# Optimization experiments

Measured on AMD Instinct MI355X. Metric: run time of the kernel, lower is better.

## Reference

```python
import jax, jax.numpy as jnp
import numpy as np

B, I, N = 1024, 128, 256
UNFOLDS = 6  # ode_solver_unfolds


def _sig(v, mu, sigma):
    # v: [B, D] -> [B, D, 1]; mu/sigma: [D, N] -> broadcast [B, D, N]
    return jax.nn.sigmoid(sigma * (v[..., None] - mu))


def setup_inputs() -> dict:
    key = jax.random.key(0)
    ks = jax.random.split(key, 12)
    u = lambda k, shape, lo, hi: jax.random.uniform(k, shape, jnp.float32, lo, hi)
    pm1 = lambda k, shape: (2.0 * jax.random.randint(k, shape, 0, 2) - 1.0).astype(jnp.float32)
    return {
        "inputs": jax.random.normal(ks[0], (B, I), jnp.float32),
        "state": jax.random.normal(ks[1], (B, N), jnp.float32) * 0.1,
        "input_w": jnp.ones((I,), jnp.float32),
        "input_b": jnp.zeros((I,), jnp.float32),
        "sensory_mu": u(ks[2], (I, N), 0.3, 0.8),
        "sensory_sigma": u(ks[3], (I, N), 3.0, 8.0),
        "sensory_W": u(ks[4], (I, N), 0.01, 1.0),
        "sensory_erev": pm1(ks[5], (I, N)),
        "mu": u(ks[6], (N, N), 0.3, 0.8),
        "sigma": u(ks[7], (N, N), 3.0, 8.0),
        "W": u(ks[8], (N, N), 0.01, 1.0),
        "erev": pm1(ks[9], (N, N)),
        "vleak": u(ks[10], (N,), -0.2, 0.2),
        "gleak": jnp.ones((N,), jnp.float32),   # gleak_init_min == gleak_init_max == 1.0
        "cm_t": jnp.full((N,), 0.5, jnp.float32),  # cm_init_min == cm_init_max == 0.5
    }


def reference(inputs, state, input_w, input_b, sensory_mu, sensory_sigma,
              sensory_W, sensory_erev, mu, sigma, W, erev, vleak, gleak, cm_t):
    # Affine input mapping
    x = inputs * input_w + input_b  # [B, I]
    # Sensory synapse activations (constant across unfolds)
    s_act = sensory_W * _sig(x, sensory_mu, sensory_sigma)  # [B, I, N]
    w_num_sensory = jnp.sum(s_act * sensory_erev, axis=1)   # [B, N]
    w_den_sensory = jnp.sum(s_act, axis=1)                  # [B, N]

    def step(v_pre, _):
        w_act = W * _sig(v_pre, mu, sigma)                  # [B, N, N]
        w_num = jnp.sum(w_act * erev, axis=1) + w_num_sensory
        w_den = jnp.sum(w_act, axis=1) + w_den_sensory
        numerator = cm_t * v_pre + gleak * vleak + w_num
        denominator = cm_t + gleak + w_den
        return numerator / denominator, None

    v_pre, _ = jax.lax.scan(step, state, None, length=UNFOLDS)
    # module returns (outputs, next_state) with outputs == next_state
    return v_pre
```

## Files before the change

kernel.cpp:

```cpp
#include <hip/hip_runtime.h>


#define LOG2E 1.44269504088896340f

constexpr int Bn = 1024;
constexpr int In = 128;
constexpr int Nn = 256;
constexpr int UNFOLDS = 6;

typedef float v2f __attribute__((ext_vector_type(2)));

#if __has_builtin(__builtin_amdgcn_exp2f)
#define EXP2F(x) __builtin_amdgcn_exp2f(x)
#else
#define EXP2F(x) __exp2f(x)
#endif
#if __has_builtin(__builtin_amdgcn_rcpf)
#define RCPF(x) __builtin_amdgcn_rcpf(x)
#else
#define RCPF(x) (1.0f / (x))
#endif

__global__ __launch_bounds__(256) void pack_kernel(
    const float* __restrict__ mu, const float* __restrict__ sigma,
    const float* __restrict__ W, const float* __restrict__ erev,
    const float* __restrict__ smu, const float* __restrict__ ssigma,
    const float* __restrict__ sW, const float* __restrict__ serev,
    float4* __restrict__ Prec, float4* __restrict__ Psen) {
    int idx = blockIdx.x * 256 + threadIdx.x;
    if (idx < Nn * Nn) {
        float s = sigma[idx], m = mu[idx], w = W[idx], e = erev[idx];
        Prec[idx] = make_float4(s * LOG2E, s * m * LOG2E, w, w * e);
        return;
    }
    int j = idx - Nn * Nn;
    if (j < In * Nn) {
        float s = ssigma[j], m = smu[j], w = sW[j], e = serev[j];
        Psen[j] = make_float4(s * LOG2E, s * m * LOG2E, w, w * e);
    }
}

__global__ __launch_bounds__(1024, 1) void ltc_fused_kernel(
    const float* __restrict__ inputs, const float* __restrict__ state,
    const float* __restrict__ input_w, const float* __restrict__ input_b,
    const float4* __restrict__ Psen, const float4* __restrict__ Prec,
    const float* __restrict__ vleak, const float* __restrict__ gleak,
    const float* __restrict__ cmt, float* __restrict__ out) {
    __shared__ float4 vt[Nn];
    __shared__ float2 part[4][4][Nn];
    __shared__ float4 xs[In];

    const int tid = threadIdx.x;
    const int b0 = blockIdx.x * 4;
    const int n = tid & 255;
    const int ih = tid >> 8;

    float vp = state[(b0 + ih) * Nn + n];
    ((float*)vt)[n * 4 + ih] = vp;
    if (tid < 4 * In) {
        int i = tid & 127, bb = tid >> 7;
        ((float*)xs)[i * 4 + bb] =
            inputs[(b0 + bb) * In + i] * input_w[i] + input_b[i];
    }
    const float g = gleak[n], c = cmt[n];
    const float gvl = g * vleak[n];
    __syncthreads();

    float sens_n, sens_d;
    {
        v2f acc0 = {0.f, 0.f}, acc1 = {0.f, 0.f};
        v2f acc2 = {0.f, 0.f}, acc3 = {0.f, 0.f};
        const float4* __restrict__ pp = Psen + n;
#pragma unroll 8
        for (int i = ih * 32; i < ih * 32 + 32; ++i) {
            float4 p = pp[i * Nn];
            float4 v = xs[i];
            v2f AA = {p.x, p.x};
            v2f BB = {p.y, p.y};
            v2f WW = {p.z, p.w};
            v2f u01 = __builtin_elementwise_fma(-AA, (v2f){v.x, v.y}, BB);
            v2f u23 = __builtin_elementwise_fma(-AA, (v2f){v.z, v.w}, BB);
            v2f a01 = (v2f){EXP2F(u01.x), EXP2F(u01.y)} + 1.0f;
            v2f a23 = (v2f){EXP2F(u23.x), EXP2F(u23.y)} + 1.0f;
            float r0 = RCPF(a01.x), r1 = RCPF(a01.y);
            float r2 = RCPF(a23.x), r3 = RCPF(a23.y);
            acc0 = __builtin_elementwise_fma(WW, (v2f){r0, r0}, acc0);
            acc1 = __builtin_elementwise_fma(WW, (v2f){r1, r1}, acc1);
            acc2 = __builtin_elementwise_fma(WW, (v2f){r2, r2}, acc2);
            acc3 = __builtin_elementwise_fma(WW, (v2f){r3, r3}, acc3);
        }
        part[ih][0][n] = make_float2(acc0.y, acc0.x);
        part[ih][1][n] = make_float2(acc1.y, acc1.x);
        part[ih][2][n] = make_float2(acc2.y, acc2.x);
        part[ih][3][n] = make_float2(acc3.y, acc3.x);
        __syncthreads();
        float wn = 0.f, wd = 0.f;
#pragma unroll
        for (int s = 0; s < 4; ++s) {
            float2 v = part[s][ih][n];
            wn += v.x;
            wd += v.y;
        }
        sens_n = wn;
        sens_d = wd;
    }

    const float4* __restrict__ pp = Prec + n;
    for (int s = 0; s < UNFOLDS; ++s) {
        __syncthreads();
        v2f acc0 = {0.f, 0.f}, acc1 = {0.f, 0.f};
        v2f acc2 = {0.f, 0.f}, acc3 = {0.f, 0.f};
#pragma unroll 8
        for (int i = ih * 64; i < ih * 64 + 64; ++i) {
            float4 p = pp[i * Nn];
            float4 v = vt[i];
            v2f AA = {p.x, p.x};
            v2f BB = {p.y, p.y};
            v2f WW = {p.z, p.w};
            v2f u01 = __builtin_elementwise_fma(-AA, (v2f){v.x, v.y}, BB);
            v2f u23 = __builtin_elementwise_fma(-AA, (v2f){v.z, v.w}, BB);
            v2f a01 = (v2f){EXP2F(u01.x), EXP2F(u01.y)} + 1.0f;
            v2f a23 = (v2f){EXP2F(u23.x), EXP2F(u23.y)} + 1.0f;
            float r0 = RCPF(a01.x), r1 = RCPF(a01.y);
            float r2 = RCPF(a23.x), r3 = RCPF(a23.y);
            acc0 = __builtin_elementwise_fma(WW, (v2f){r0, r0}, acc0);
            acc1 = __builtin_elementwise_fma(WW, (v2f){r1, r1}, acc1);
            acc2 = __builtin_elementwise_fma(WW, (v2f){r2, r2}, acc2);
            acc3 = __builtin_elementwise_fma(WW, (v2f){r3, r3}, acc3);
        }
        part[ih][0][n] = make_float2(acc0.y, acc0.x);
        part[ih][1][n] = make_float2(acc1.y, acc1.x);
        part[ih][2][n] = make_float2(acc2.y, acc2.x);
        part[ih][3][n] = make_float2(acc3.y, acc3.x);
        __syncthreads();
        float wn = sens_n, wd = sens_d;
#pragma unroll
        for (int s2 = 0; s2 < 4; ++s2) {
            float2 v = part[s2][ih][n];
            wn += v.x;
            wd += v.y;
        }
        float res = (c * vp + gvl + wn) * RCPF(c + g + wd);
        vp = res;
        if (s == UNFOLDS - 1)
            out[(b0 + ih) * Nn + n] = res;
        else
            ((float*)vt)[n * 4 + ih] = res;
    }
}

extern "C" void kernel_launch(void* const* d_in, const int* in_sizes, int n_in,
                              void* d_out, int out_size, void* d_ws, size_t ws_size,
                              hipStream_t stream) {
    const float* inputs   = (const float*)d_in[0];
    const float* state    = (const float*)d_in[1];
    const float* input_w  = (const float*)d_in[2];
    const float* input_b  = (const float*)d_in[3];
    const float* smu      = (const float*)d_in[4];
    const float* ssigma   = (const float*)d_in[5];
    const float* sW       = (const float*)d_in[6];
    const float* serev    = (const float*)d_in[7];
    const float* mu       = (const float*)d_in[8];
    const float* sigma    = (const float*)d_in[9];
    const float* W        = (const float*)d_in[10];
    const float* erev     = (const float*)d_in[11];
    const float* vleak    = (const float*)d_in[12];
    const float* gleak    = (const float*)d_in[13];
    const float* cmt      = (const float*)d_in[14];
    float* out = (float*)d_out;

    char* ws = (char*)d_ws;
    float4* Prec = (float4*)ws;
    float4* Psen = (float4*)(ws + (1u << 20));

    pack_kernel<<<(Nn * Nn + In * Nn + 255) / 256, 256, 0, stream>>>(
        mu, sigma, W, erev, smu, ssigma, sW, serev, Prec, Psen);

    ltc_fused_kernel<<<Bn / 4, 1024, 0, stream>>>(
        inputs, state, input_w, input_b, Psen, Prec, vleak, gleak, cmt, out);
}
```

Before: 172.5 us.

## Replace LDS partial-sum reduction with wave shuffles and double-buffer state

Each wavefront now holds 16 neurons times 4 input-quarter slices, so the cross-slice reduction runs through __shfl_xor within a wave instead of a shared-memory partial array plus an extra barrier. The state vector is double-buffered and padded, which leaves one barrier per unfold step instead of two. The cost is more shuffle instructions, and global loads of the packed parameters become less contiguous per wave: 16 consecutive n per i-row instead of 64.

```diff
diff --git a/kernel.cpp b/kernel.cpp
--- a/kernel.cpp
+++ b/kernel.cpp
@@ -20,6 +20,10 @@
 #else
 #define RCPF(x) (1.0f / (x))
 #endif
+
+__device__ __forceinline__ v2f shfl_xor2(v2f x, int m) {
+    return (v2f){__shfl_xor(x.x, m, 64), __shfl_xor(x.y, m, 64)};
+}
 
 __global__ __launch_bounds__(256) void pack_kernel(
     const float* __restrict__ mu, const float* __restrict__ sigma,
@@ -46,35 +50,38 @@
     const float4* __restrict__ Psen, const float4* __restrict__ Prec,
     const float* __restrict__ vleak, const float* __restrict__ gleak,
     const float* __restrict__ cmt, float* __restrict__ out) {
-    __shared__ float4 vt[Nn];
-    __shared__ float2 part[4][4][Nn];
-    __shared__ float4 xs[In];
+    __shared__ float4 vt[2][260];
+    __shared__ float4 xs[132];
 
-    const int tid = threadIdx.x;
-    const int b0 = blockIdx.x * 4;
-    const int n = tid & 255;
-    const int ih = tid >> 8;
+    const int tid  = threadIdx.x;
+    const int b0   = blockIdx.x * 4;
+    const int lane = tid & 63;
+    const int w    = tid >> 6;
+    const int nl   = lane & 15;
+    const int ih   = lane >> 4;
+    const int n    = w * 16 + nl;
 
     float vp = state[(b0 + ih) * Nn + n];
-    ((float*)vt)[n * 4 + ih] = vp;
-    if (tid < 4 * In) {
+    ((float*)&vt[0][n + (n >> 6)])[ih] = vp;
+    if (tid < 512) {
         int i = tid & 127, bb = tid >> 7;
-        ((float*)xs)[i * 4 + bb] =
+        ((float*)&xs[i + (i >> 5)])[bb] =
             inputs[(b0 + bb) * In + i] * input_w[i] + input_b[i];
     }
     const float g = gleak[n], c = cmt[n];
     const float gvl = g * vleak[n];
     __syncthreads();
 
-    float sens_n, sens_d;
+    v2f sens;
     {
         v2f acc0 = {0.f, 0.f}, acc1 = {0.f, 0.f};
         v2f acc2 = {0.f, 0.f}, acc3 = {0.f, 0.f};
         const float4* __restrict__ pp = Psen + n;
 #pragma unroll 8
-        for (int i = ih * 32; i < ih * 32 + 32; ++i) {
+        for (int ii = 0; ii < 32; ++ii) {
+            int i = ih * 32 + ii;
             float4 p = pp[i * Nn];
-            float4 v = xs[i];
+            float4 v = xs[i + ih];
             v2f AA = {p.x, p.x};
             v2f BB = {p.y, p.y};
             v2f WW = {p.z, p.w};
@@ -89,31 +96,28 @@
             acc2 = __builtin_elementwise_fma(WW, (v2f){r2, r2}, acc2);
             acc3 = __builtin_elementwise_fma(WW, (v2f){r3, r3}, acc3);
         }
-        part[ih][0][n] = make_float2(acc0.y, acc0.x);
-        part[ih][1][n] = make_float2(acc1.y, acc1.x);
-        part[ih][2][n] = make_float2(acc2.y, acc2.x);
-        part[ih][3][n] = make_float2(acc3.y, acc3.x);
-        __syncthreads();
-        float wn = 0.f, wd = 0.f;
-#pragma unroll
-        for (int s = 0; s < 4; ++s) {
-            float2 v = part[s][ih][n];
-            wn += v.x;
-            wd += v.y;
-        }
-        sens_n = wn;
-        sens_d = wd;
+        acc0 += shfl_xor2(acc0, 16);
+        acc1 += shfl_xor2(acc1, 16);
+        acc2 += shfl_xor2(acc2, 16);
+        acc3 += shfl_xor2(acc3, 16);
+        acc0 += shfl_xor2(acc0, 32);
+        acc1 += shfl_xor2(acc1, 32);
+        acc2 += shfl_xor2(acc2, 32);
+        acc3 += shfl_xor2(acc3, 32);
+        sens = (ih == 0) ? acc0 : (ih == 1) ? acc1 : (ih == 2) ? acc2 : acc3;
     }
 
     const float4* __restrict__ pp = Prec + n;
+    int cur = 0;
     for (int s = 0; s < UNFOLDS; ++s) {
-        __syncthreads();
         v2f acc0 = {0.f, 0.f}, acc1 = {0.f, 0.f};
         v2f acc2 = {0.f, 0.f}, acc3 = {0.f, 0.f};
+        const float4* __restrict__ vc = vt[cur];
 #pragma unroll 8
-        for (int i = ih * 64; i < ih * 64 + 64; ++i) {
+        for (int ii = 0; ii < 64; ++ii) {
+            int i = ih * 64 + ii;
             float4 p = pp[i * Nn];
-            float4 v = vt[i];
+            float4 v = vc[i + ih];
             v2f AA = {p.x, p.x};
             v2f BB = {p.y, p.y};
             v2f WW = {p.z, p.w};
@@ -128,24 +132,27 @@
             acc2 = __builtin_elementwise_fma(WW, (v2f){r2, r2}, acc2);
             acc3 = __builtin_elementwise_fma(WW, (v2f){r3, r3}, acc3);
         }
-        part[ih][0][n] = make_float2(acc0.y, acc0.x);
-        part[ih][1][n] = make_float2(acc1.y, acc1.x);
-        part[ih][2][n] = make_float2(acc2.y, acc2.x);
-        part[ih][3][n] = make_float2(acc3.y, acc3.x);
-        __syncthreads();
-        float wn = sens_n, wd = sens_d;
-#pragma unroll
-        for (int s2 = 0; s2 < 4; ++s2) {
-            float2 v = part[s2][ih][n];
-            wn += v.x;
-            wd += v.y;
-        }
+        acc0 += shfl_xor2(acc0, 16);
+        acc1 += shfl_xor2(acc1, 16);
+        acc2 += shfl_xor2(acc2, 16);
+        acc3 += shfl_xor2(acc3, 16);
+        acc0 += shfl_xor2(acc0, 32);
+        acc1 += shfl_xor2(acc1, 32);
+        acc2 += shfl_xor2(acc2, 32);
+        acc3 += shfl_xor2(acc3, 32);
+        v2f a = (ih == 0) ? acc0 : (ih == 1) ? acc1 : (ih == 2) ? acc2 : acc3;
+
+        float wn = sens.y + a.y;
+        float wd = sens.x + a.x;
         float res = (c * vp + gvl + wn) * RCPF(c + g + wd);
         vp = res;
-        if (s == UNFOLDS - 1)
+        if (s == UNFOLDS - 1) {
             out[(b0 + ih) * Nn + n] = res;
-        else
-            ((float*)vt)[n * 4 + ih] = res;
+        } else {
+            ((float*)&vt[cur ^ 1][n + (n >> 6)])[ih] = res;
+            __syncthreads();
+        }
+        cur ^= 1;
     }
 }
 
```

Measured after the change: 173.1 us. About the same (+0.3%).
